# Kernel tuning notes

Measured on AMD Instinct MI355X. Metric: run time of the kernel, lower is better.

Reference implementation:

```python
import jax, jax.numpy as jnp
import numpy as np

E = 32      # num_embodiments
A = 64      # action_dim
H = 1024    # hidden_size
B = 64
T = 64


def setup_inputs() -> dict:
    key = jax.random.key(0)
    ks = jax.random.split(key, 9)
    return {
        "actions": jax.random.normal(ks[0], (B, T, A), dtype=jnp.float32),
        "W1_W": 0.02 * jax.random.normal(ks[1], (E, A, H), dtype=jnp.float32),
        "W1_b": jnp.zeros((E, H), dtype=jnp.float32),
        "W2_W": 0.02 * jax.random.normal(ks[2], (E, 2 * H, H), dtype=jnp.float32),
        "W2_b": jnp.zeros((E, H), dtype=jnp.float32),
        "W3_W": 0.02 * jax.random.normal(ks[3], (E, H, H), dtype=jnp.float32),
        "W3_b": jnp.zeros((E, H), dtype=jnp.float32),
        "timesteps": jax.random.randint(ks[4], (B,), 0, 1000, dtype=jnp.int32),
        "cat_ids": jax.random.randint(ks[5], (B,), 0, E, dtype=jnp.int32),
    }


def _cat_linear(x, W, b, cat_ids):
    # x: (B,T,in), W: (E,in,out), b: (E,out)
    Wg = W[cat_ids]               # (B,in,out) gathered per-batch weights
    bg = b[cat_ids]               # (B,out)
    return jnp.einsum('bti,bio->bto', x, Wg) + bg[:, None, :]


def _sinusoidal_pe(t, dim):
    # t: (B,T) float -> (B,T,dim)
    half = dim // 2
    exponent = -jnp.arange(half, dtype=jnp.float32) * (jnp.log(jnp.float32(10000.0)) / half)
    freqs = t[..., None] * jnp.exp(exponent)
    return jnp.concatenate([jnp.sin(freqs), jnp.cos(freqs)], axis=-1)


def reference(actions, W1_W, W1_b, W2_W, W2_b, W3_W, W3_b, timesteps, cat_ids):
    b, t, _ = actions.shape
    ts = jnp.broadcast_to(timesteps.astype(jnp.float32)[:, None], (b, t))  # (B,T)
    a_emb = _cat_linear(actions, W1_W, W1_b, cat_ids)                      # (B,T,H)
    tau_emb = _sinusoidal_pe(ts, H).astype(a_emb.dtype)                    # (B,T,H)
    x = jnp.concatenate([a_emb, tau_emb], axis=-1)                         # (B,T,2H)
    h = _cat_linear(x, W2_W, W2_b, cat_ids)
    x = h * jax.nn.sigmoid(h)                                              # swish
    return _cat_linear(x, W3_W, W3_b, cat_ids)                             # (B,T,H)
```

## Files before the change

### kernel.cpp

```cpp
#include <hip/hip_runtime.h>
#include <hip/hip_bf16.h>

#define NB 64
#define NT 64
#define NA 64
#define NH 1024
#define NE 32
#define K2DIM 2048

typedef unsigned short bf16_t;
typedef __attribute__((ext_vector_type(8))) short bf16x8;
typedef __attribute__((ext_vector_type(4))) float f32x4;

__device__ __forceinline__ float bf16_lo(unsigned int u) {
    return __uint_as_float(u << 16);
}
__device__ __forceinline__ float bf16_hi(unsigned int u) {
    return __uint_as_float(u & 0xFFFF0000u);
}
__device__ __forceinline__ bf16_t f32_to_bf16(float f) {
    unsigned int u = __float_as_uint(f);
    u = (u + 0x7FFFu + ((u >> 16) & 1u)) >> 16;
    return (bf16_t)u;
}
__device__ __forceinline__ unsigned int pack_bf16x2(float lo, float hi) {
    return (unsigned int)f32_to_bf16(lo) | ((unsigned int)f32_to_bf16(hi) << 16);
}

__global__ __launch_bounds__(256) void k1_embed(
    const float* __restrict__ actions, const float* __restrict__ W1,
    const float* __restrict__ b1, const int* __restrict__ timesteps,
    const int* __restrict__ cat_ids, bf16_t* __restrict__ x)
{
    __shared__ float act[NT][NA];
    __shared__ float pe[64];

    const int b   = blockIdx.x;
    const int c0  = blockIdx.y * 64;
    const int tid = threadIdx.x;
    const int cat = cat_ids[b];
    const float ts = (float)timesteps[b];

    const float* ab = actions + b * (NT * NA);
    #pragma unroll
    for (int p = 0; p < 16; ++p) {
        int idx = tid + p * 256;
        act[idx >> 6][idx & 63] = ab[idx];
    }
    if (tid < 64) {
        const float kfreq = logf(10000.0f) / 512.0f;
        int c = c0 + tid;
        float v;
        if (c < 512) v = sinf(ts * expf(-(float)c * kfreq));
        else         v = cosf(ts * expf(-(float)(c - 512) * kfreq));
        pe[tid] = v;
    }
    __syncthreads();

    const int cc = tid & 63;
    const int c  = c0 + cc;
    const int t0 = tid >> 6;

    float acc[16];
    const float bias = b1[cat * NH + c];
    #pragma unroll
    for (int i = 0; i < 16; ++i) acc[i] = bias;

    const float* Wp = W1 + (size_t)cat * (NA * NH) + c;
    #pragma unroll 8
    for (int k = 0; k < NA; ++k) {
        float w = Wp[(size_t)k * NH];
        #pragma unroll
        for (int i = 0; i < 16; ++i)
            acc[i] = fmaf(act[t0 + 4 * i][k], w, acc[i]);
    }

    bf16_t* xb = x + (size_t)b * (NT * K2DIM);
    const bf16_t pv = f32_to_bf16(pe[cc]);
    #pragma unroll
    for (int i = 0; i < 16; ++i) {
        int t = t0 + 4 * i;
        xb[(size_t)t * K2DIM + c]      = f32_to_bf16(acc[i]);
        xb[(size_t)t * K2DIM + NH + c] = pv;
    }
}

template<int KDIM, bool SWISH, typename OutT>
__global__ __launch_bounds__(256, 4) void gemm_mfma(
    const bf16_t* __restrict__ xin, const float* __restrict__ W,
    const float* __restrict__ bias, const int* __restrict__ cat_ids,
    OutT* __restrict__ out)
{
    __shared__ char xs[64 * 128];
    __shared__ char wsm[64 * 128];

    const int b    = blockIdx.x;
    const int n0   = blockIdx.y * 64;
    const int tid  = threadIdx.x;
    const int lane = tid & 63;
    const int wv   = tid >> 6;
    const int cat  = cat_ids[b];

    const int mw = (wv & 1) * 32;
    const int nw = (wv >> 1) * 32;
    const int l15 = lane & 15;
    const int l4  = lane >> 4;

    const bf16_t* xb = xin + (size_t)b * (size_t)NT * KDIM;
    const float*  Wb = W + (size_t)cat * KDIM * NH + n0;

    f32x4 acc[2][2];
    #pragma unroll
    for (int m = 0; m < 2; ++m)
        #pragma unroll
        for (int n = 0; n < 2; ++n) {
            float bv = bias[(size_t)cat * NH + n0 + nw + n * 16 + l15];
            acc[m][n] = (f32x4){bv, bv, bv, bv};
        }

    const int nn   = lane;
    const int wswz = (nn & 7) << 4;

    for (int kc = 0; kc < KDIM / 64; ++kc) {
        const bf16_t* xsrc = xb + kc * 64;
        const float*  Wp   = Wb + (size_t)(kc * 64) * NH;

        __syncthreads();

        #pragma unroll
        for (int p = 0; p < 2; ++p) {
            int id = tid + p * 256;
            int t  = id >> 3;
            int k8 = id & 7;
            uint4 v = *(const uint4*)(xsrc + (size_t)t * KDIM + k8 * 8);
            int off = (t * 128 + k8 * 16) ^ ((t & 7) << 4);
            *(uint4*)(xs + off) = v;
        }
        #pragma unroll
        for (int p = 0; p < 8; ++p) {
            int k0 = 2 * (p * 4 + wv);
            float a0 = Wp[(size_t)k0 * NH + nn];
            float a1 = Wp[(size_t)(k0 + 1) * NH + nn];
            unsigned int pk = pack_bf16x2(a0, a1);
            int off = (nn * 128 + k0 * 2) ^ wswz;
            *(unsigned int*)(wsm + off) = pk;
        }
        __syncthreads();

        #pragma unroll
        for (int ks = 0; ks < 2; ++ks) {
            bf16x8 af[2], bfr[2];
            #pragma unroll
            for (int m = 0; m < 2; ++m) {
                int row = mw + m * 16 + l15;
                int off = (row * 128 + ks * 64 + l4 * 16) ^ ((row & 7) << 4);
                af[m] = *(const bf16x8*)(xs + off);
            }
            #pragma unroll
            for (int n = 0; n < 2; ++n) {
                int row = nw + n * 16 + l15;
                int off = (row * 128 + ks * 64 + l4 * 16) ^ ((row & 7) << 4);
                bfr[n] = *(const bf16x8*)(wsm + off);
            }
            #pragma unroll
            for (int m = 0; m < 2; ++m)
                #pragma unroll
                for (int n = 0; n < 2; ++n)
                    acc[m][n] = __builtin_amdgcn_mfma_f32_16x16x32_bf16(
                        af[m], bfr[n], acc[m][n], 0, 0, 0);
        }
    }

    #pragma unroll
    for (int m = 0; m < 2; ++m) {
        #pragma unroll
        for (int n = 0; n < 2; ++n) {
            int col = n0 + nw + n * 16 + l15;
            #pragma unroll
            for (int r = 0; r < 4; ++r) {
                int row = mw + m * 16 + l4 * 4 + r;
                float h = acc[m][n][r];
                if (SWISH) h = h / (1.0f + __expf(-h));
                if constexpr (sizeof(OutT) == 2) {
                    out[((size_t)b * NT + row) * NH + col] = (OutT)f32_to_bf16(h);
                } else {
                    out[((size_t)b * NT + row) * NH + col] = h;
                }
            }
        }
    }
}

extern "C" void kernel_launch(void* const* d_in, const int* in_sizes, int n_in,
                              void* d_out, int out_size, void* d_ws, size_t ws_size,
                              hipStream_t stream) {
    const float* actions   = (const float*)d_in[0];
    const float* W1        = (const float*)d_in[1];
    const float* b1        = (const float*)d_in[2];
    const float* W2        = (const float*)d_in[3];
    const float* b2        = (const float*)d_in[4];
    const float* W3        = (const float*)d_in[5];
    const float* b3        = (const float*)d_in[6];
    const int*   timesteps = (const int*)d_in[7];
    const int*   cat_ids   = (const int*)d_in[8];
    float* out = (float*)d_out;

    bf16_t* x = (bf16_t*)d_ws;
    bf16_t* y = x + (size_t)NB * NT * K2DIM;

    k1_embed<<<dim3(NB, NH / 64), 256, 0, stream>>>(actions, W1, b1, timesteps, cat_ids, x);
    gemm_mfma<K2DIM, true,  bf16_t><<<dim3(NB, NH / 64), 256, 0, stream>>>(x, W2, b2, cat_ids, y);
    gemm_mfma<NH,    false, float ><<<dim3(NB, NH / 64), 256, 0, stream>>>(y, W3, b3, cat_ids, out);
}
```

Baseline: 179.1 us.

## Widen GEMM N tile to 128, vectorize weight loads, use transposed LDS reads

Each GEMM block now covers 128 output columns instead of 64, so every staged activation tile feeds twice as many MFMAs and the grid halves. Weights are loaded as float4 pairs along N, converted to bf16 and stored row-major in LDS, and then read with ds_read_b64_tr_b16 to build the K-major B fragments. The old path used scalar strided loads and manual packing. Per-thread accumulator count doubles and occupancy bounds drop to 2 blocks per CU, which reduces parallelism across the 64-batch grid.

```diff
diff --git a/kernel.cpp b/kernel.cpp
--- a/kernel.cpp
+++ b/kernel.cpp
@@ -10,21 +10,18 @@
 
 typedef unsigned short bf16_t;
 typedef __attribute__((ext_vector_type(8))) short bf16x8;
+typedef __attribute__((ext_vector_type(4))) short s16x4;
 typedef __attribute__((ext_vector_type(4))) float f32x4;
 
-__device__ __forceinline__ float bf16_lo(unsigned int u) {
-    return __uint_as_float(u << 16);
-}
-__device__ __forceinline__ float bf16_hi(unsigned int u) {
-    return __uint_as_float(u & 0xFFFF0000u);
-}
 __device__ __forceinline__ bf16_t f32_to_bf16(float f) {
     unsigned int u = __float_as_uint(f);
     u = (u + 0x7FFFu + ((u >> 16) & 1u)) >> 16;
     return (bf16_t)u;
 }
-__device__ __forceinline__ unsigned int pack_bf16x2(float lo, float hi) {
-    return (unsigned int)f32_to_bf16(lo) | ((unsigned int)f32_to_bf16(hi) << 16);
+__device__ __forceinline__ unsigned cvt2(float x, float y) {
+    unsigned short a = __builtin_bit_cast(unsigned short, __float2bfloat16(x));
+    unsigned short b = __builtin_bit_cast(unsigned short, __float2bfloat16(y));
+    return (unsigned)a | ((unsigned)b << 16);
 }
 
 __global__ __launch_bounds__(256) void k1_embed(
@@ -86,40 +83,40 @@
 }
 
 template<int KDIM, bool SWISH, typename OutT>
-__global__ __launch_bounds__(256, 4) void gemm_mfma(
+__global__ __launch_bounds__(256, 2) void gemm_mfma(
     const bf16_t* __restrict__ xin, const float* __restrict__ W,
     const float* __restrict__ bias, const int* __restrict__ cat_ids,
     OutT* __restrict__ out)
 {
-    __shared__ char xs[64 * 128];
-    __shared__ char wsm[64 * 128];
+    __shared__ __align__(128) char xs[64 * 128];
+    __shared__ __align__(128) char wsm[16384];
 
     const int b    = blockIdx.x;
-    const int n0   = blockIdx.y * 64;
+    const int n0   = blockIdx.y * 128;
     const int tid  = threadIdx.x;
     const int lane = tid & 63;
     const int wv   = tid >> 6;
     const int cat  = cat_ids[b];
 
     const int mw = (wv & 1) * 32;
-    const int nw = (wv >> 1) * 32;
+    const int nw = (wv >> 1) * 64;
+    const int pw = (wv >> 1) * 4;
     const int l15 = lane & 15;
     const int l4  = lane >> 4;
 
     const bf16_t* xb = xin + (size_t)b * (size_t)NT * KDIM;
     const float*  Wb = W + (size_t)cat * KDIM * NH + n0;
 
-    f32x4 acc[2][2];
-    #pragma unroll
-    for (int m = 0; m < 2; ++m)
-        #pragma unroll
-        for (int n = 0; n < 2; ++n) {
-            float bv = bias[(size_t)cat * NH + n0 + nw + n * 16 + l15];
-            acc[m][n] = (f32x4){bv, bv, bv, bv};
-        }
-
-    const int nn   = lane;
-    const int wswz = (nn & 7) << 4;
+    f32x4 acc[2][4];
+    #pragma unroll
+    for (int nf = 0; nf < 4; ++nf) {
+        float bv = bias[(size_t)cat * NH + n0 + nw + nf * 16 + l15];
+        acc[0][nf] = (f32x4){bv, bv, bv, bv};
+        acc[1][nf] = acc[0][nf];
+    }
+
+    const unsigned wbase = (unsigned)(unsigned long long)&wsm[0];
+    const unsigned laneB = wbase + (unsigned)(l4 * 2048 + l15 * 8);
 
     for (int kc = 0; kc < KDIM / 64; ++kc) {
         const bf16_t* xsrc = xb + kc * 64;
@@ -137,49 +134,61 @@
             *(uint4*)(xs + off) = v;
         }
         #pragma unroll
-        for (int p = 0; p < 8; ++p) {
-            int k0 = 2 * (p * 4 + wv);
-            float a0 = Wp[(size_t)k0 * NH + nn];
-            float a1 = Wp[(size_t)(k0 + 1) * NH + nn];
-            unsigned int pk = pack_bf16x2(a0, a1);
-            int off = (nn * 128 + k0 * 2) ^ wswz;
-            *(unsigned int*)(wsm + off) = pk;
+        for (int p = 0; p < 4; ++p) {
+            int id  = tid + p * 256;
+            int k   = id >> 4;
+            int oct = id & 15;
+            const float* src = Wp + (size_t)k * NH + oct * 8;
+            float4 w0 = *(const float4*)(src);
+            float4 w1 = *(const float4*)(src + 4);
+            uint4 pk;
+            pk.x = cvt2(w0.x, w0.y);
+            pk.y = cvt2(w0.z, w0.w);
+            pk.z = cvt2(w1.x, w1.y);
+            pk.w = cvt2(w1.z, w1.w);
+            int off = ((k >> 2) * 8 + (oct >> 1)) * 128 + (k & 3) * 32 + (oct & 1) * 16;
+            *(uint4*)(wsm + off) = pk;
         }
         __syncthreads();
 
         #pragma unroll
         for (int ks = 0; ks < 2; ++ks) {
-            bf16x8 af[2], bfr[2];
+            bf16x8 af[2];
             #pragma unroll
             for (int m = 0; m < 2; ++m) {
                 int row = mw + m * 16 + l15;
                 int off = (row * 128 + ks * 64 + l4 * 16) ^ ((row & 7) << 4);
                 af[m] = *(const bf16x8*)(xs + off);
             }
-            #pragma unroll
-            for (int n = 0; n < 2; ++n) {
-                int row = nw + n * 16 + l15;
-                int off = (row * 128 + ks * 64 + l4 * 16) ^ ((row & 7) << 4);
-                bfr[n] = *(const bf16x8*)(wsm + off);
+            bf16x8 bfr[4];
+            #pragma unroll
+            for (int nf = 0; nf < 4; ++nf) {
+                unsigned a = laneB + (unsigned)(ks * 8192 + (pw + nf) * 128);
+                s16x4 lo, hi;
+                asm volatile("ds_read_b64_tr_b16 %0, %1" : "=v"(lo) : "v"(a));
+                asm volatile("ds_read_b64_tr_b16 %0, %1 offset:1024" : "=v"(hi) : "v"(a));
+                bfr[nf] = __builtin_shufflevector(lo, hi, 0, 1, 2, 3, 4, 5, 6, 7);
             }
+            asm volatile("s_waitcnt lgkmcnt(0)" ::: "memory");
+            __builtin_amdgcn_sched_barrier(0);
             #pragma unroll
             for (int m = 0; m < 2; ++m)
                 #pragma unroll
-                for (int n = 0; n < 2; ++n)
-                    acc[m][n] = __builtin_amdgcn_mfma_f32_16x16x32_bf16(
-                        af[m], bfr[n], acc[m][n], 0, 0, 0);
+                for (int nf = 0; nf < 4; ++nf)
+                    acc[m][nf] = __builtin_amdgcn_mfma_f32_16x16x32_bf16(
+                        af[m], bfr[nf], acc[m][nf], 0, 0, 0);
         }
     }
 
     #pragma unroll
     for (int m = 0; m < 2; ++m) {
         #pragma unroll
-        for (int n = 0; n < 2; ++n) {
-            int col = n0 + nw + n * 16 + l15;
+        for (int nf = 0; nf < 4; ++nf) {
+            int col = n0 + nw + nf * 16 + l15;
             #pragma unroll
             for (int r = 0; r < 4; ++r) {
                 int row = mw + m * 16 + l4 * 4 + r;
-                float h = acc[m][n][r];
+                float h = acc[m][nf][r];
                 if (SWISH) h = h / (1.0f + __expf(-h));
                 if constexpr (sizeof(OutT) == 2) {
                     out[((size_t)b * NT + row) * NH + col] = (OutT)f32_to_bf16(h);
@@ -209,6 +218,6 @@
     bf16_t* y = x + (size_t)NB * NT * K2DIM;
 
     k1_embed<<<dim3(NB, NH / 64), 256, 0, stream>>>(actions, W1, b1, timesteps, cat_ids, x);
-    gemm_mfma<K2DIM, true,  bf16_t><<<dim3(NB, NH / 64), 256, 0, stream>>>(x, W2, b2, cat_ids, y);
-    gemm_mfma<NH,    false, float ><<<dim3(NB, NH / 64), 256, 0, stream>>>(y, W3, b3, cat_ids, out);
-}
+    gemm_mfma<K2DIM, true,  bf16_t><<<dim3(NB, NH / 128), 256, 0, stream>>>(x, W2, b2, cat_ids, y);
+    gemm_mfma<NH,    false, float ><<<dim3(NB, NH / 128), 256, 0, stream>>>(y, W3, b3, cat_ids, out);
+}
```

Result: faster. 157.5 us (-12.1%).
